# Performance work log

Measured on AMD Instinct MI355X. Metric: run time of the kernel, lower is better.

## Reference

```python
import jax, jax.numpy as jnp
import numpy as np

B, N, C_IN, L, C_OUT = 8, 50000, 32, 9, 64
M, NNZ = 12500, 37500


def setup_inputs() -> dict:
    key = jax.random.key(0)
    k = jax.random.split(key, 7)
    x = jax.random.normal(k[0], (B, N, C_IN), dtype=jnp.float32)
    weight = jax.random.normal(k[1], (L * C_IN, C_OUT), dtype=jnp.float32) * (1.0 / np.sqrt(L * C_IN))
    bias = jax.random.normal(k[2], (C_OUT,), dtype=jnp.float32) * 0.01
    values = jax.random.uniform(k[3], (NNZ,), dtype=jnp.float32)
    spiral_indices = jax.random.randint(k[4], (N, L), 0, N, dtype=jnp.int64)
    rows = jax.random.randint(k[5], (NNZ,), 0, M, dtype=jnp.int64)
    cols = jax.random.randint(k[6], (NNZ,), 0, N, dtype=jnp.int64)
    return {"x": x, "weight": weight, "bias": bias, "values": values,
            "spiral_indices": spiral_indices, "rows": rows, "cols": cols,
            "num_out_verts": M}


def reference(x, weight, bias, values, spiral_indices, rows, cols, num_out_verts):
    b, n, c = x.shape
    # SpiralConv: gather spiral neighborhoods, flatten, linear
    g = x[:, spiral_indices]                      # [B, N, L, C]
    g = g.reshape(b, n, -1)                       # [B, N, L*C]
    out = jnp.einsum('bnk,ko->bno', g, weight) + bias
    out = jax.nn.elu(out)                         # [B, N, C_OUT]
    # Pool: sparse down_transform (gather, scale, scatter_add)
    gathered = out[:, cols] * values[None, :, None]          # [B, NNZ, C_OUT]
    pooled = jnp.zeros((b, num_out_verts, out.shape[-1]), dtype=out.dtype)
    pooled = pooled.at[:, rows].add(gathered)                # [B, M, C_OUT]
    return pooled
```

## Files before the change

kernel.cpp:

```cpp
#include <hip/hip_runtime.h>

#define BATCH   8
#define NVERT   50000
#define CIN     32
#define LSP     9
#define COUT    64
#define MVERT   12500
#define NNZ     37500

#define NFRAG   2304
#define OUTDW   (BATCH * MVERT * COUT)

#define TILE_T  128
#define TPB     293

#define PRE_BLOCKS   6250
#define PACK_BLOCKS  9
#define ZERO_BLOCKS  6250

#define SORT_BLOCKS  49
#define SORT_THREADS (SORT_BLOCKS * 256)

typedef __attribute__((ext_vector_type(8))) short  short8;
typedef __attribute__((ext_vector_type(4))) float  floatx4;

static __device__ __forceinline__ unsigned short f2bf(float f) {
    union { float f; unsigned int u; } c; c.f = f;
    unsigned int u = c.u;
    return (unsigned short)((u + 0x7fffu + ((u >> 16) & 1u)) >> 16);
}

__device__ int g_bsum[64];
__device__ int g_bsumP[64];

__global__ __launch_bounds__(256)
void prep_kernel(const float* __restrict__ x, const float* __restrict__ w,
                 unsigned short* __restrict__ x16, unsigned short* __restrict__ wp,
                 float* __restrict__ out, int* __restrict__ barcnt)
{
    const int blk = blockIdx.x;
    const int tid = threadIdx.x;
    if (blk < PRE_BLOCKS) {
        const size_t base = ((size_t)blk * 256 + tid) * 8;
        const float4* s = (const float4*)(x + base);
        float4 a = s[0], c = s[1];
        unsigned short t[8];
        t[0]=f2bf(a.x); t[1]=f2bf(a.y); t[2]=f2bf(a.z); t[3]=f2bf(a.w);
        t[4]=f2bf(c.x); t[5]=f2bf(c.y); t[6]=f2bf(c.z); t[7]=f2bf(c.w);
        *(uint4*)(x16 + base) = *(uint4*)t;
    } else if (blk < PRE_BLOCKS + PACK_BLOCKS) {
        const int f = (blk - PRE_BLOCKS) * 256 + tid;
        if (f < NFRAG) {
            int s = f >> 8, g = (f >> 6) & 3, lane = f & 63;
            int k0 = s * 32 + (lane >> 4) * 8, col = g * 16 + (lane & 15);
            unsigned short t[8];
            #pragma unroll
            for (int j = 0; j < 8; ++j)
                t[j] = f2bf(w[(size_t)(k0 + j) * COUT + col]);
            ((uint4*)wp)[f] = *(uint4*)t;
        }
    } else {
        if (blk == PRE_BLOCKS + PACK_BLOCKS && tid == 0) *barcnt = 0;
        const size_t base = ((size_t)(blk - PRE_BLOCKS - PACK_BLOCKS) * 256 + tid) * 4;
        if (base < OUTDW) *(uint4*)(out + base) = (uint4){0, 0, 0, 0};
    }
}

static __device__ __forceinline__ void gbar(int* cnt, int target) {
    __syncthreads();
    if (threadIdx.x == 0) {
        __hip_atomic_fetch_add(cnt, 1, __ATOMIC_RELEASE, __HIP_MEMORY_SCOPE_AGENT);
        while (__hip_atomic_load(cnt, __ATOMIC_ACQUIRE, __HIP_MEMORY_SCOPE_AGENT) < target)
            __builtin_amdgcn_s_sleep(2);
    }
    __syncthreads();
}

__global__ __launch_bounds__(256)
void sort_kernel(const int* __restrict__ rows, const int* __restrict__ cols,
                 const float* __restrict__ vals, const int* __restrict__ spiral,
                 int* __restrict__ hist, int* __restrict__ off2,
                 int* __restrict__ rows_s, float* __restrict__ vals_s,
                 unsigned short* __restrict__ tidx, int* __restrict__ barcnt)
{
    const int blk = blockIdx.x;
    const int tid = threadIdx.x;
    const int gid = blk * 256 + tid;

    if (gid < MVERT) hist[gid] = 0;
    gbar(barcnt, 1 * SORT_BLOCKS);

    for (int z = gid; z < NNZ; z += SORT_THREADS)
        atomicAdd(&hist[rows[z]], 1);
    gbar(barcnt, 2 * SORT_BLOCKS);

    __shared__ int sh[256];
    {
        const int v = (gid < MVERT) ? hist[gid] : 0;
        sh[tid] = v;
        __syncthreads();
        #pragma unroll
        for (int d = 1; d < 256; d <<= 1) {
            int u = (tid >= d) ? sh[tid - d] : 0;
            __syncthreads();
            sh[tid] += u;
            __syncthreads();
        }
        const int incl = sh[tid];
        if (gid < MVERT) off2[gid] = incl - v;
        if (tid == 255) g_bsum[blk] = incl;
    }
    gbar(barcnt, 3 * SORT_BLOCKS);

    if (blk == 0 && tid == 0) {
        int run = 0;
        for (int k = 0; k < SORT_BLOCKS; ++k) {
            int t = g_bsum[k];
            g_bsumP[k] = run;
            run += t;
        }
    }
    gbar(barcnt, 4 * SORT_BLOCKS);

    if (gid < MVERT) off2[gid] += g_bsumP[blk];
    gbar(barcnt, 5 * SORT_BLOCKS);

    for (int z = gid; z < NNZ; z += SORT_THREADS) {
        int r = rows[z];
        int c = cols[z];
        int pos = atomicAdd(&off2[r], 1);
        rows_s[pos] = r;
        vals_s[pos] = vals[z];
        unsigned short t[16];
        #pragma unroll
        for (int s = 0; s < 9; ++s) t[s] = (unsigned short)spiral[c * LSP + s];
        #pragma unroll
        for (int s = 9; s < 16; ++s) t[s] = 0;
        uint4* dst = (uint4*)(tidx + (size_t)pos * 16);
        dst[0] = *(uint4*)t;
        dst[1] = *(uint4*)(t + 8);
    }
}

__global__ __launch_bounds__(256, 4)
void spiral_mfma9_kernel(const unsigned short* __restrict__ x16,
                         const unsigned short* __restrict__ wp,
                         const float* __restrict__ bias,
                         const unsigned short* __restrict__ tidx,
                         const int* __restrict__ rows_s,
                         const float* __restrict__ vals_s,
                         float* __restrict__ out)
{
    const int bid  = blockIdx.x;
    const int b    = bid & 7;
    const int tile = bid >> 3;
    const int tid  = threadIdx.x;
    const int w    = tid >> 6;
    const int lane = tid & 63;
    const int quad = lane >> 4;
    const int m16  = lane & 15;
    const int z0w  = tile * TILE_T + 32 * w;

    const int   zc   = min(z0w + (lane & 31), NNZ - 1);
    const int   rowv = rows_s[zc];
    const float valv = vals_s[zc];
    const uint4 p0 = *(const uint4*)(tidx + (size_t)zc * 16);
    const unsigned int p1 = *(const unsigned int*)(tidx + (size_t)zc * 16 + 8);
    int idx[9];
    idx[0] = p0.x & 0xffff;  idx[1] = p0.x >> 16;
    idx[2] = p0.y & 0xffff;  idx[3] = p0.y >> 16;
    idx[4] = p0.z & 0xffff;  idx[5] = p0.z >> 16;
    idx[6] = p0.w & 0xffff;  idx[7] = p0.w >> 16;
    idx[8] = p1 & 0xffff;

    const unsigned short* xb = x16 + (size_t)b * NVERT * CIN;

    short8 A[2][9];
    #pragma unroll
    for (int s = 0; s < 9; ++s) {
        #pragma unroll
        for (int mt = 0; mt < 2; ++mt) {
            int tix = __shfl(idx[s], mt * 16 + m16);
            A[mt][s] = *(const short8*)(xb + (size_t)tix * CIN + quad * 8);
        }
    }

    floatx4 acc[2][4];
    #pragma unroll
    for (int mt = 0; mt < 2; ++mt)
        #pragma unroll
        for (int g = 0; g < 4; ++g) acc[mt][g] = (floatx4){0.f, 0.f, 0.f, 0.f};

    #pragma unroll
    for (int s = 0; s < 9; ++s) {
        short8 bf[4];
        #pragma unroll
        for (int g = 0; g < 4; ++g)
            bf[g] = *(const short8*)(wp + (size_t)((s * 4 + g) * 64 + lane) * 8);
        #pragma unroll
        for (int mt = 0; mt < 2; ++mt)
            #pragma unroll
            for (int g = 0; g < 4; ++g)
                acc[mt][g] = __builtin_amdgcn_mfma_f32_16x16x32_bf16(A[mt][s], bf[g], acc[mt][g], 0, 0, 0);
    }

    float bs[4];
    #pragma unroll
    for (int g = 0; g < 4; ++g) bs[g] = bias[g * 16 + m16];
    float* outb = out + (size_t)b * MVERT * COUT;

    #pragma unroll
    for (int mt = 0; mt < 2; ++mt) {
        int   rr[4]; float vv[4]; bool val[4];
        #pragma unroll
        for (int r = 0; r < 4; ++r) {
            const int tsk = mt * 16 + quad * 4 + r;
            rr[r]  = __shfl(rowv, tsk);
            vv[r]  = __shfl(valv, tsk);
            val[r] = (z0w + tsk) < NNZ;
        }
        bool emit[4];
        #pragma unroll
        for (int r = 0; r < 4; ++r)
            emit[r] = (r == 3) || (!val[r + 1 > 3 ? 3 : r + 1]) || (rr[r + 1 > 3 ? 3 : r + 1] != rr[r]);
        #pragma unroll
        for (int g = 0; g < 4; ++g) {
            const int ch = g * 16 + m16;
            float s = 0.0f;
            #pragma unroll
            for (int r = 0; r < 4; ++r) {
                if (val[r]) {
                    float y = acc[mt][g][r] + bs[g];
                    y = (y > 0.0f) ? y : (__expf(y) - 1.0f);
                    s += y * vv[r];
                    if (emit[r]) {
                        atomicAdd(outb + (size_t)rr[r] * COUT + ch, s);
                        s = 0.0f;
                    }
                }
            }
        }
    }
}

extern "C" void kernel_launch(void* const* d_in, const int* in_sizes, int n_in,
                              void* d_out, int out_size, void* d_ws, size_t ws_size,
                              hipStream_t stream) {
    const float* x      = (const float*)d_in[0];
    const float* w      = (const float*)d_in[1];
    const float* bias   = (const float*)d_in[2];
    const float* vals   = (const float*)d_in[3];
    const int*   spiral = (const int*)d_in[4];
    const int*   rows   = (const int*)d_in[5];
    const int*   cols   = (const int*)d_in[6];
    float* out = (float*)d_out;

    char* base = (char*)d_ws;
    unsigned short* wp     = (unsigned short*)(base);
    unsigned short* x16    = (unsigned short*)(base + 36864);
    int*            hist   = (int*)(base + 25636864);
    int*            off2   = (int*)(base + 25686864);
    int*            rows_s = (int*)(base + 25736864);
    int*            barcnt = (int*)(base + 25900000);
    float*          vals_s = (float*)(base + 26036896);
    unsigned short* tidx   = (unsigned short*)(base + 26186912);

    const int prep_grid = PRE_BLOCKS + PACK_BLOCKS + ZERO_BLOCKS;
    prep_kernel<<<prep_grid, 256, 0, stream>>>(x, w, x16, wp, out, barcnt);
    sort_kernel<<<SORT_BLOCKS, 256, 0, stream>>>(rows, cols, vals, spiral,
                                                 hist, off2, rows_s, vals_s,
                                                 tidx, barcnt);
    spiral_mfma9_kernel<<<BATCH * TPB, 256, 0, stream>>>(x16, wp, bias, tidx,
                                                         rows_s, vals_s, out);
}
```

Baseline: 187.2 us.

## Fuse sort into prep kernel and shrink MFMA tiles to 16 tasks per wave

The sort stage now runs as the first 49 blocks of the prep kernel instead of as its own launch, so it overlaps with the bf16 conversion and zeroing work. The histogram and barrier counter are cleared with a memset beforehand, which removes one grid-barrier phase. The spiral MFMA kernel now gives each wave a single 16-row tile instead of two, using fewer registers (launch bounds raised to 5) and launching twice as many blocks. The risk is that the grid barrier depends on the 49 sort blocks being co-resident while thousands of other blocks are scheduled, and that halving the tile doubles how often the weight fragments are loaded.

```diff
diff --git a/kernel.cpp b/kernel.cpp
--- a/kernel.cpp
+++ b/kernel.cpp
@@ -11,15 +11,14 @@
 #define NFRAG   2304
 #define OUTDW   (BATCH * MVERT * COUT)
 
-#define TILE_T  128
-#define TPB     293
-
+#define TASKS_PB 64
+#define BLK_B    586
+
+#define SORT_BLOCKS  49
+#define SORT_THREADS (SORT_BLOCKS * 256)
 #define PRE_BLOCKS   6250
 #define PACK_BLOCKS  9
 #define ZERO_BLOCKS  6250
-
-#define SORT_BLOCKS  49
-#define SORT_THREADS (SORT_BLOCKS * 256)
 
 typedef __attribute__((ext_vector_type(8))) short  short8;
 typedef __attribute__((ext_vector_type(4))) float  floatx4;
@@ -33,23 +32,97 @@
 __device__ int g_bsum[64];
 __device__ int g_bsumP[64];
 
+static __device__ __forceinline__ void gbar(int* cnt, int target) {
+    __syncthreads();
+    if (threadIdx.x == 0) {
+        __hip_atomic_fetch_add(cnt, 1, __ATOMIC_RELEASE, __HIP_MEMORY_SCOPE_AGENT);
+        while (__hip_atomic_load(cnt, __ATOMIC_ACQUIRE, __HIP_MEMORY_SCOPE_AGENT) < target)
+            __builtin_amdgcn_s_sleep(2);
+    }
+    __syncthreads();
+}
+
 __global__ __launch_bounds__(256)
-void prep_kernel(const float* __restrict__ x, const float* __restrict__ w,
-                 unsigned short* __restrict__ x16, unsigned short* __restrict__ wp,
-                 float* __restrict__ out, int* __restrict__ barcnt)
+void prep_sort_kernel(const float* __restrict__ x, const float* __restrict__ w,
+                      const int* __restrict__ rows, const int* __restrict__ cols,
+                      const float* __restrict__ vals, const int* __restrict__ spiral,
+                      unsigned short* __restrict__ x16, unsigned short* __restrict__ wp,
+                      float* __restrict__ out,
+                      int* __restrict__ hist, int* __restrict__ barcnt,
+                      int* __restrict__ off2,
+                      int* __restrict__ rows_s, float* __restrict__ vals_s,
+                      unsigned short* __restrict__ tidx)
 {
     const int blk = blockIdx.x;
     const int tid = threadIdx.x;
-    if (blk < PRE_BLOCKS) {
-        const size_t base = ((size_t)blk * 256 + tid) * 8;
+
+    if (blk < SORT_BLOCKS) {
+        const int gid = blk * 256 + tid;
+
+        for (int z = gid; z < NNZ; z += SORT_THREADS)
+            atomicAdd(&hist[rows[z]], 1);
+        gbar(barcnt, 1 * SORT_BLOCKS);
+
+        __shared__ int sh[256];
+        {
+            const int v = (gid < MVERT) ? hist[gid] : 0;
+            sh[tid] = v;
+            __syncthreads();
+            #pragma unroll
+            for (int d = 1; d < 256; d <<= 1) {
+                int u = (tid >= d) ? sh[tid - d] : 0;
+                __syncthreads();
+                sh[tid] += u;
+                __syncthreads();
+            }
+            const int incl = sh[tid];
+            if (gid < MVERT) off2[gid] = incl - v;
+            if (tid == 255) g_bsum[blk] = incl;
+        }
+        gbar(barcnt, 2 * SORT_BLOCKS);
+
+        if (blk == 0 && tid == 0) {
+            int run = 0;
+            for (int k = 0; k < SORT_BLOCKS; ++k) {
+                int t = g_bsum[k];
+                g_bsumP[k] = run;
+                run += t;
+            }
+        }
+        gbar(barcnt, 3 * SORT_BLOCKS);
+
+        if (gid < MVERT) off2[gid] += g_bsumP[blk];
+        gbar(barcnt, 4 * SORT_BLOCKS);
+
+        for (int z = gid; z < NNZ; z += SORT_THREADS) {
+            int r = rows[z];
+            int c = cols[z];
+            int pos = atomicAdd(&off2[r], 1);
+            rows_s[pos] = r;
+            vals_s[pos] = vals[z];
+            unsigned short t[16];
+            #pragma unroll
+            for (int s = 0; s < 9; ++s) t[s] = (unsigned short)spiral[c * LSP + s];
+            #pragma unroll
+            for (int s = 9; s < 16; ++s) t[s] = 0;
+            uint4* dst = (uint4*)(tidx + (size_t)pos * 16);
+            dst[0] = *(uint4*)t;
+            dst[1] = *(uint4*)(t + 8);
+        }
+        return;
+    }
+
+    const int pblk = blk - SORT_BLOCKS;
+    if (pblk < PRE_BLOCKS) {
+        const size_t base = ((size_t)pblk * 256 + tid) * 8;
         const float4* s = (const float4*)(x + base);
         float4 a = s[0], c = s[1];
         unsigned short t[8];
         t[0]=f2bf(a.x); t[1]=f2bf(a.y); t[2]=f2bf(a.z); t[3]=f2bf(a.w);
         t[4]=f2bf(c.x); t[5]=f2bf(c.y); t[6]=f2bf(c.z); t[7]=f2bf(c.w);
         *(uint4*)(x16 + base) = *(uint4*)t;
-    } else if (blk < PRE_BLOCKS + PACK_BLOCKS) {
-        const int f = (blk - PRE_BLOCKS) * 256 + tid;
+    } else if (pblk < PRE_BLOCKS + PACK_BLOCKS) {
+        const int f = (pblk - PRE_BLOCKS) * 256 + tid;
         if (f < NFRAG) {
             int s = f >> 8, g = (f >> 6) & 3, lane = f & 63;
             int k0 = s * 32 + (lane >> 4) * 8, col = g * 16 + (lane & 15);
@@ -60,96 +133,19 @@
             ((uint4*)wp)[f] = *(uint4*)t;
         }
     } else {
-        if (blk == PRE_BLOCKS + PACK_BLOCKS && tid == 0) *barcnt = 0;
-        const size_t base = ((size_t)(blk - PRE_BLOCKS - PACK_BLOCKS) * 256 + tid) * 4;
+        const size_t base = ((size_t)(pblk - PRE_BLOCKS - PACK_BLOCKS) * 256 + tid) * 4;
         if (base < OUTDW) *(uint4*)(out + base) = (uint4){0, 0, 0, 0};
     }
 }
 
-static __device__ __forceinline__ void gbar(int* cnt, int target) {
-    __syncthreads();
-    if (threadIdx.x == 0) {
-        __hip_atomic_fetch_add(cnt, 1, __ATOMIC_RELEASE, __HIP_MEMORY_SCOPE_AGENT);
-        while (__hip_atomic_load(cnt, __ATOMIC_ACQUIRE, __HIP_MEMORY_SCOPE_AGENT) < target)
-            __builtin_amdgcn_s_sleep(2);
-    }
-    __syncthreads();
-}
-
-__global__ __launch_bounds__(256)
-void sort_kernel(const int* __restrict__ rows, const int* __restrict__ cols,
-                 const float* __restrict__ vals, const int* __restrict__ spiral,
-                 int* __restrict__ hist, int* __restrict__ off2,
-                 int* __restrict__ rows_s, float* __restrict__ vals_s,
-                 unsigned short* __restrict__ tidx, int* __restrict__ barcnt)
-{
-    const int blk = blockIdx.x;
-    const int tid = threadIdx.x;
-    const int gid = blk * 256 + tid;
-
-    if (gid < MVERT) hist[gid] = 0;
-    gbar(barcnt, 1 * SORT_BLOCKS);
-
-    for (int z = gid; z < NNZ; z += SORT_THREADS)
-        atomicAdd(&hist[rows[z]], 1);
-    gbar(barcnt, 2 * SORT_BLOCKS);
-
-    __shared__ int sh[256];
-    {
-        const int v = (gid < MVERT) ? hist[gid] : 0;
-        sh[tid] = v;
-        __syncthreads();
-        #pragma unroll
-        for (int d = 1; d < 256; d <<= 1) {
-            int u = (tid >= d) ? sh[tid - d] : 0;
-            __syncthreads();
-            sh[tid] += u;
-            __syncthreads();
-        }
-        const int incl = sh[tid];
-        if (gid < MVERT) off2[gid] = incl - v;
-        if (tid == 255) g_bsum[blk] = incl;
-    }
-    gbar(barcnt, 3 * SORT_BLOCKS);
-
-    if (blk == 0 && tid == 0) {
-        int run = 0;
-        for (int k = 0; k < SORT_BLOCKS; ++k) {
-            int t = g_bsum[k];
-            g_bsumP[k] = run;
-            run += t;
-        }
-    }
-    gbar(barcnt, 4 * SORT_BLOCKS);
-
-    if (gid < MVERT) off2[gid] += g_bsumP[blk];
-    gbar(barcnt, 5 * SORT_BLOCKS);
-
-    for (int z = gid; z < NNZ; z += SORT_THREADS) {
-        int r = rows[z];
-        int c = cols[z];
-        int pos = atomicAdd(&off2[r], 1);
-        rows_s[pos] = r;
-        vals_s[pos] = vals[z];
-        unsigned short t[16];
-        #pragma unroll
-        for (int s = 0; s < 9; ++s) t[s] = (unsigned short)spiral[c * LSP + s];
-        #pragma unroll
-        for (int s = 9; s < 16; ++s) t[s] = 0;
-        uint4* dst = (uint4*)(tidx + (size_t)pos * 16);
-        dst[0] = *(uint4*)t;
-        dst[1] = *(uint4*)(t + 8);
-    }
-}
-
-__global__ __launch_bounds__(256, 4)
-void spiral_mfma9_kernel(const unsigned short* __restrict__ x16,
-                         const unsigned short* __restrict__ wp,
-                         const float* __restrict__ bias,
-                         const unsigned short* __restrict__ tidx,
-                         const int* __restrict__ rows_s,
-                         const float* __restrict__ vals_s,
-                         float* __restrict__ out)
+__global__ __launch_bounds__(256, 5)
+void spiral_mfma10_kernel(const unsigned short* __restrict__ x16,
+                          const unsigned short* __restrict__ wp,
+                          const float* __restrict__ bias,
+                          const unsigned short* __restrict__ tidx,
+                          const int* __restrict__ rows_s,
+                          const float* __restrict__ vals_s,
+                          float* __restrict__ out)
 {
     const int bid  = blockIdx.x;
     const int b    = bid & 7;
@@ -159,9 +155,9 @@
     const int lane = tid & 63;
     const int quad = lane >> 4;
     const int m16  = lane & 15;
-    const int z0w  = tile * TILE_T + 32 * w;
-
-    const int   zc   = min(z0w + (lane & 31), NNZ - 1);
+    const int z0w  = tile * TASKS_PB + 16 * w;
+
+    const int   zc   = min(z0w + m16, NNZ - 1);
     const int   rowv = rows_s[zc];
     const float valv = vals_s[zc];
     const uint4 p0 = *(const uint4*)(tidx + (size_t)zc * 16);
@@ -175,21 +171,16 @@
 
     const unsigned short* xb = x16 + (size_t)b * NVERT * CIN;
 
-    short8 A[2][9];
+    short8 A[9];
     #pragma unroll
     for (int s = 0; s < 9; ++s) {
-        #pragma unroll
-        for (int mt = 0; mt < 2; ++mt) {
-            int tix = __shfl(idx[s], mt * 16 + m16);
-            A[mt][s] = *(const short8*)(xb + (size_t)tix * CIN + quad * 8);
-        }
-    }
-
-    floatx4 acc[2][4];
-    #pragma unroll
-    for (int mt = 0; mt < 2; ++mt)
-        #pragma unroll
-        for (int g = 0; g < 4; ++g) acc[mt][g] = (floatx4){0.f, 0.f, 0.f, 0.f};
+        int tix = __shfl(idx[s], m16);
+        A[s] = *(const short8*)(xb + (size_t)tix * CIN + quad * 8);
+    }
+
+    floatx4 acc[4];
+    #pragma unroll
+    for (int g = 0; g < 4; ++g) acc[g] = (floatx4){0.f, 0.f, 0.f, 0.f};
 
     #pragma unroll
     for (int s = 0; s < 9; ++s) {
@@ -198,10 +189,8 @@
         for (int g = 0; g < 4; ++g)
             bf[g] = *(const short8*)(wp + (size_t)((s * 4 + g) * 64 + lane) * 8);
         #pragma unroll
-        for (int mt = 0; mt < 2; ++mt)
-            #pragma unroll
-            for (int g = 0; g < 4; ++g)
-                acc[mt][g] = __builtin_amdgcn_mfma_f32_16x16x32_bf16(A[mt][s], bf[g], acc[mt][g], 0, 0, 0);
+        for (int g = 0; g < 4; ++g)
+            acc[g] = __builtin_amdgcn_mfma_f32_16x16x32_bf16(A[s], bf[g], acc[g], 0, 0, 0);
     }
 
     float bs[4];
@@ -209,34 +198,31 @@
     for (int g = 0; g < 4; ++g) bs[g] = bias[g * 16 + m16];
     float* outb = out + (size_t)b * MVERT * COUT;
 
-    #pragma unroll
-    for (int mt = 0; mt < 2; ++mt) {
-        int   rr[4]; float vv[4]; bool val[4];
+    int   rr[4]; float vv[4]; bool val[4];
+    #pragma unroll
+    for (int r = 0; r < 4; ++r) {
+        const int tsk = quad * 4 + r;
+        rr[r]  = __shfl(rowv, tsk);
+        vv[r]  = __shfl(valv, tsk);
+        val[r] = (z0w + tsk) < NNZ;
+    }
+    bool emit[4];
+    #pragma unroll
+    for (int r = 0; r < 4; ++r)
+        emit[r] = (r == 3) || (!val[r + 1 > 3 ? 3 : r + 1]) || (rr[r + 1 > 3 ? 3 : r + 1] != rr[r]);
+    #pragma unroll
+    for (int g = 0; g < 4; ++g) {
+        const int ch = g * 16 + m16;
+        float s = 0.0f;
         #pragma unroll
         for (int r = 0; r < 4; ++r) {
-            const int tsk = mt * 16 + quad * 4 + r;
-            rr[r]  = __shfl(rowv, tsk);
-            vv[r]  = __shfl(valv, tsk);
-            val[r] = (z0w + tsk) < NNZ;
-        }
-        bool emit[4];
-        #pragma unroll
-        for (int r = 0; r < 4; ++r)
-            emit[r] = (r == 3) || (!val[r + 1 > 3 ? 3 : r + 1]) || (rr[r + 1 > 3 ? 3 : r + 1] != rr[r]);
-        #pragma unroll
-        for (int g = 0; g < 4; ++g) {
-            const int ch = g * 16 + m16;
-            float s = 0.0f;
-            #pragma unroll
-            for (int r = 0; r < 4; ++r) {
-                if (val[r]) {
-                    float y = acc[mt][g][r] + bs[g];
-                    y = (y > 0.0f) ? y : (__expf(y) - 1.0f);
-                    s += y * vv[r];
-                    if (emit[r]) {
-                        atomicAdd(outb + (size_t)rr[r] * COUT + ch, s);
-                        s = 0.0f;
-                    }
+            if (val[r]) {
+                float y = acc[g][r] + bs[g];
+                y = (y > 0.0f) ? y : (__expf(y) - 1.0f);
+                s += y * vv[r];
+                if (emit[r]) {
+                    atomicAdd(outb + (size_t)rr[r] * COUT + ch, s);
+                    s = 0.0f;
                 }
             }
         }
@@ -259,17 +245,19 @@
     unsigned short* wp     = (unsigned short*)(base);
     unsigned short* x16    = (unsigned short*)(base + 36864);
     int*            hist   = (int*)(base + 25636864);
-    int*            off2   = (int*)(base + 25686864);
-    int*            rows_s = (int*)(base + 25736864);
-    int*            barcnt = (int*)(base + 25900000);
-    float*          vals_s = (float*)(base + 26036896);
+    int*            barcnt = (int*)(base + 25686864);
+    int*            off2   = (int*)(base + 25686880);
+    int*            rows_s = (int*)(base + 25736880);
+    float*          vals_s = (float*)(base + 25886880);
     unsigned short* tidx   = (unsigned short*)(base + 26186912);
 
-    const int prep_grid = PRE_BLOCKS + PACK_BLOCKS + ZERO_BLOCKS;
-    prep_kernel<<<prep_grid, 256, 0, stream>>>(x, w, x16, wp, out, barcnt);
-    sort_kernel<<<SORT_BLOCKS, 256, 0, stream>>>(rows, cols, vals, spiral,
-                                                 hist, off2, rows_s, vals_s,
-                                                 tidx, barcnt);
-    spiral_mfma9_kernel<<<BATCH * TPB, 256, 0, stream>>>(x16, wp, bias, tidx,
-                                                         rows_s, vals_s, out);
-}
+    hipMemsetAsync(hist, 0, MVERT * sizeof(int) + 16, stream);
+
+    const int fused_grid = SORT_BLOCKS + PRE_BLOCKS + PACK_BLOCKS + ZERO_BLOCKS;
+    prep_sort_kernel<<<fused_grid, 256, 0, stream>>>(x, w, rows, cols, vals,
+                                                     spiral, x16, wp, out,
+                                                     hist, barcnt, off2,
+                                                     rows_s, vals_s, tidx);
+    spiral_mfma10_kernel<<<BATCH * BLK_B, 256, 0, stream>>>(x16, wp, bias, tidx,
+                                                            rows_s, vals_s, out);
+}
```

New measurement: 186.0 us. About the same (-0.7%).
